# Optimization experiments

Hardware: AMD Instinct MI355X
Metric: run time of the kernel (lower is better)

Reference implementation:

```python
import jax, jax.numpy as jnp
import numpy as np

NUM_HEAD = 8

def conv1x1(x, W, b):
    # x: (n, c, h, w); W: (o, c); b: (o,)
    return jnp.einsum('nchw,oc->nohw', x, W) + b[None, :, None, None]

def setup_inputs() -> dict:
    key = jax.random.key(0)
    ks = jax.random.split(key, 9)
    n, C, H, Wd = 16, 512, 64, 64
    KC, VC = 256, 512
    s = lambda fan_in: 1.0 / np.sqrt(fan_in)
    return {
        'x':  jax.random.normal(ks[0], (n, C, H, Wd), dtype=jnp.float32),
        'Wk': jax.random.normal(ks[1], (KC, C), dtype=jnp.float32) * s(C),
        'bk': jnp.zeros((KC,), dtype=jnp.float32),
        'Wq': jax.random.normal(ks[2], (KC, C), dtype=jnp.float32) * s(C),
        'bq': jnp.zeros((KC,), dtype=jnp.float32),
        'Wv': jax.random.normal(ks[3], (VC, C), dtype=jnp.float32) * s(C),
        'bv': jnp.zeros((VC,), dtype=jnp.float32),
        'We': jax.random.normal(ks[4], (C, VC), dtype=jnp.float32) * s(VC),
        'be': jnp.zeros((C,), dtype=jnp.float32),
    }

def reference(x, Wk, bk, Wq, bq, Wv, bv, We, be):
    n, c, h, w = x.shape
    L = h * w
    Hn = NUM_HEAD
    key   = conv1x1(x, Wk, bk).reshape(n, Hn, -1, L)   # (n, H, hk, L)
    query = conv1x1(x, Wq, bq).reshape(n, Hn, -1, L)   # (n, H, hk, L)
    value = conv1x1(x, Wv, bv).reshape(n, Hn, -1, L)   # (n, H, hv, L)
    key_sm   = jax.nn.softmax(key, axis=3)              # softmax over spatial
    query_sm = jax.nn.softmax(query, axis=2)            # softmax over head channels
    # linear attention: (value @ key^T) @ query, no LxL matrix
    context = jnp.einsum('nhvl,nhkl->nhvk', value, key_sm)     # (n, H, hv, hk)
    att = jnp.einsum('nhvk,nhkl->nhvl', context, query_sm)     # (n, H, hv, L)
    att = att.reshape(n, -1, h, w)                              # (n, VC, h, w)
    return x + conv1x1(att, We, be)
```

## Files before the change

kernel.cpp:

```cpp
#include <hip/hip_runtime.h>
#include <cstddef>
#include <cstdint>

#define N_BATCH 16
#define C_IN    512
#define L       4096
#define KC      256
#define VC      512
#define NH      8
#define HK      32
#define HV      64

using f32x4 = __attribute__((ext_vector_type(4))) float;
using s16x8 = __attribute__((ext_vector_type(8))) short;

static __device__ inline ushort f2bf(float f) {
  uint32_t u = __float_as_uint(f);
  uint32_t r = (u + 0x7FFFu + ((u >> 16) & 1u)) >> 16;
  return (ushort)r;
}
static __device__ inline float bf2f(ushort u) {
  return __uint_as_float((uint32_t)u << 16);
}

__global__ __launch_bounds__(256) void k_prep_w(
    const float* __restrict__ Wk, const float* __restrict__ bk,
    const float* __restrict__ Wq, const float* __restrict__ bq,
    ushort* __restrict__ Wb, float* __restrict__ bb)
{
  const int o = blockIdx.x;
  const float* src; const float* bsrc; int oo;
  if (o < 256) { src = Wk + (size_t)o * C_IN;         bsrc = bk; oo = o; }
  else         { src = Wq + (size_t)(o - 256) * C_IN; bsrc = bq; oo = o - 256; }
  const int t = threadIdx.x;
  Wb[(size_t)o * C_IN + t * 2]     = f2bf(src[t * 2]);
  Wb[(size_t)o * C_IN + t * 2 + 1] = f2bf(src[t * 2 + 1]);
  if (t == 0) bb[o] = bsrc[oo];
}

__global__ __launch_bounds__(256) void k_prep_x(const float* __restrict__ x,
                                                ushort* __restrict__ xT)
{
  __shared__ float t[64][65];
  const int n = blockIdx.z, cy = blockIdx.y, lx = blockIdx.x;
  const float* xp = x + ((size_t)n * C_IN + cy * 64) * L + (size_t)lx * 64;
  const int l4 = (threadIdx.x & 15) * 4;
  const int c0 = threadIdx.x >> 4;
  #pragma unroll
  for (int i = 0; i < 4; ++i) {
    int cc = c0 + i * 16;
    f32x4 v = *(const f32x4*)&xp[(size_t)cc * L + l4];
    t[cc][l4]     = v[0];
    t[cc][l4 + 1] = v[1];
    t[cc][l4 + 2] = v[2];
    t[cc][l4 + 3] = v[3];
  }
  __syncthreads();
  ushort* op = xT + ((size_t)n * L + lx * 64) * C_IN + cy * 64;
  const int cp = (threadIdx.x & 15) * 4;
  const int l0 = threadIdx.x >> 4;
  #pragma unroll
  for (int i = 0; i < 4; ++i) {
    int lr = l0 + i * 16;
    uint2 pk;
    pk.x = (uint32_t)f2bf(t[cp][lr])     | ((uint32_t)f2bf(t[cp + 1][lr]) << 16);
    pk.y = (uint32_t)f2bf(t[cp + 2][lr]) | ((uint32_t)f2bf(t[cp + 3][lr]) << 16);
    *(uint2*)(op + (size_t)lr * C_IN + cp) = pk;
  }
}

#define QBM 256
#define QBN 256
#define QBK 64

__global__ __launch_bounds__(512) void k_kq_mfma(
    const ushort* __restrict__ Wb,
    const ushort* __restrict__ xT,
    const float* __restrict__ bb,
    ushort* __restrict__ Kbuf,
    ushort* __restrict__ qT)
{
  extern __shared__ __align__(16) char smem[];
  const int n  = blockIdx.z;
  const int oy = blockIdx.y;
  const int lx = blockIdx.x;
  const int tid  = threadIdx.x;
  const int wave = tid >> 6, lane = tid & 63;
  const int wr = wave >> 2, wc = wave & 3;

  f32x4 acc[8][4] = {};

  const ushort* gA = Wb + (size_t)(oy * QBM) * C_IN;
  const ushort* gB = xT + ((size_t)n * L + lx * QBN) * C_IN;

  const int srow = lane >> 3;
  const int sslotbase = lane & 7;

  #define QSTAGE(buf, k0)                                                        \
    {                                                                            \
      ushort* As_ = (ushort*)(smem + (buf) * 65536);                             \
      ushort* Bs_ = (ushort*)(smem + (buf) * 65536 + 32768);                     \
      _Pragma("unroll")                                                          \
      for (int i_ = 0; i_ < 4; ++i_) {                                           \
        int rbase_ = wave * 32 + i_ * 8;                                         \
        int row_ = rbase_ + srow;                                                \
        int ss_ = sslotbase ^ (row_ & 7);                                        \
        __builtin_amdgcn_global_load_lds(                                        \
            (const __attribute__((address_space(1))) uint32_t*)(gA + (size_t)row_ * C_IN + (k0) + ss_ * 8), \
            (__attribute__((address_space(3))) uint32_t*)(As_ + rbase_ * QBK),   \
            16, 0, 0);                                                           \
        __builtin_amdgcn_global_load_lds(                                        \
            (const __attribute__((address_space(1))) uint32_t*)(gB + (size_t)row_ * C_IN + (k0) + ss_ * 8), \
            (__attribute__((address_space(3))) uint32_t*)(Bs_ + rbase_ * QBK),   \
            16, 0, 0);                                                           \
      }                                                                          \
    }

  QSTAGE(0, 0)
  __syncthreads();

  const int nt = C_IN / QBK;
  for (int t = 0; t < nt; ++t) {
    if (t < nt - 1) QSTAGE((t + 1) & 1, (t + 1) * QBK)
    ushort* As = (ushort*)(smem + (t & 1) * 65536);
    ushort* Bs = (ushort*)(smem + (t & 1) * 65536 + 32768);
    __builtin_amdgcn_s_setprio(1);
    #pragma unroll
    for (int ks = 0; ks < 2; ++ks) {
      s16x8 af[8], bfr[4];
      #pragma unroll
      for (int m = 0; m < 8; ++m) {
        int row = wr * 128 + m * 16 + (lane & 15);
        int slot = (ks * 4 + (lane >> 4)) ^ (row & 7);
        af[m] = *(const s16x8*)&As[row * QBK + slot * 8];
      }
      #pragma unroll
      for (int nn = 0; nn < 4; ++nn) {
        int row = wc * 64 + nn * 16 + (lane & 15);
        int slot = (ks * 4 + (lane >> 4)) ^ (row & 7);
        bfr[nn] = *(const s16x8*)&Bs[row * QBK + slot * 8];
      }
      #pragma unroll
      for (int m = 0; m < 8; ++m)
        #pragma unroll
        for (int nn = 0; nn < 4; ++nn)
          acc[m][nn] = __builtin_amdgcn_mfma_f32_16x16x32_bf16(af[m], bfr[nn], acc[m][nn], 0, 0, 0);
    }
    __builtin_amdgcn_s_setprio(0);
    __syncthreads();
  }
  #undef QSTAGE

  if (oy == 0) {
    float* ep = (float*)smem + wave * (16 * 68);
    const int erow = lane >> 4;
    const int ecol = lane & 15;
    const float* bias = bb + wr * 128;
    ushort* outp = Kbuf + ((size_t)n * 256 + wr * 128) * L
                 + (size_t)lx * QBN + wc * 64;
    #pragma unroll
    for (int m = 0; m < 8; ++m) {
      #pragma unroll
      for (int nn = 0; nn < 4; ++nn)
        #pragma unroll
        for (int r = 0; r < 4; ++r)
          ep[(erow * 4 + r) * 68 + nn * 16 + ecol] = acc[m][nn][r];
      #pragma unroll
      for (int p = 0; p < 4; ++p) {
        int row = p * 4 + erow;
        f32x4 v = *(const f32x4*)&ep[row * 68 + ecol * 4];
        float bo = bias[m * 16 + row];
        uint2 pk;
        pk.x = (uint32_t)f2bf(v[0] + bo) | ((uint32_t)f2bf(v[1] + bo) << 16);
        pk.y = (uint32_t)f2bf(v[2] + bo) | ((uint32_t)f2bf(v[3] + bo) << 16);
        *(uint2*)&outp[(size_t)(m * 16 + row) * L + ecol * 4] = pk;
      }
    }
  } else {
    const float* bias = bb + 256 + wr * 128;
    ushort* qbase = qT + (size_t)n * L * KC;
    const int g4 = (lane >> 4) * 4;
    #pragma unroll
    for (int hp = 0; hp < 4; ++hp) {
      const int m0 = 2 * hp, m1 = 2 * hp + 1;
      const float b0_0 = bias[m0 * 16 + g4 + 0], b0_1 = bias[m0 * 16 + g4 + 1];
      const float b0_2 = bias[m0 * 16 + g4 + 2], b0_3 = bias[m0 * 16 + g4 + 3];
      const float b1_0 = bias[m1 * 16 + g4 + 0], b1_1 = bias[m1 * 16 + g4 + 1];
      const float b1_2 = bias[m1 * 16 + g4 + 2], b1_3 = bias[m1 * 16 + g4 + 3];
      #pragma unroll
      for (int nn = 0; nn < 4; ++nn) {
        float v0[4], v1[4];
        v0[0] = acc[m0][nn][0] + b0_0; v0[1] = acc[m0][nn][1] + b0_1;
        v0[2] = acc[m0][nn][2] + b0_2; v0[3] = acc[m0][nn][3] + b0_3;
        v1[0] = acc[m1][nn][0] + b1_0; v1[1] = acc[m1][nn][1] + b1_1;
        v1[2] = acc[m1][nn][2] + b1_2; v1[3] = acc[m1][nn][3] + b1_3;
        float mx = fmaxf(fmaxf(fmaxf(v0[0], v0[1]), fmaxf(v0[2], v0[3])),
                         fmaxf(fmaxf(v1[0], v1[1]), fmaxf(v1[2], v1[3])));
        mx = fmaxf(mx, __shfl_xor(mx, 16));
        mx = fmaxf(mx, __shfl_xor(mx, 32));
        float e0[4], e1[4];
        float s = 0.f;
        #pragma unroll
        for (int r = 0; r < 4; ++r) { e0[r] = __expf(v0[r] - mx); s += e0[r]; }
        #pragma unroll
        for (int r = 0; r < 4; ++r) { e1[r] = __expf(v1[r] - mx); s += e1[r]; }
        s += __shfl_xor(s, 16);
        s += __shfl_xor(s, 32);
        float inv = 1.0f / s;
        int l = lx * QBN + wc * 64 + nn * 16 + (lane & 15);
        ushort* dst = qbase + (size_t)l * KC + wr * 128;
        uint2 p0, p1;
        p0.x = (uint32_t)f2bf(e0[0] * inv) | ((uint32_t)f2bf(e0[1] * inv) << 16);
        p0.y = (uint32_t)f2bf(e0[2] * inv) | ((uint32_t)f2bf(e0[3] * inv) << 16);
        p1.x = (uint32_t)f2bf(e1[0] * inv) | ((uint32_t)f2bf(e1[1] * inv) << 16);
        p1.y = (uint32_t)f2bf(e1[2] * inv) | ((uint32_t)f2bf(e1[3] * inv) << 16);
        *(uint2*)&dst[m0 * 16 + g4] = p0;
        *(uint2*)&dst[m1 * 16 + g4] = p1;
      }
    }
  }
}

__device__ inline float blockReduceMax(float v, float* red) {
  #pragma unroll
  for (int off = 32; off > 0; off >>= 1)
    v = fmaxf(v, __shfl_down(v, off, 64));
  int tid = threadIdx.x;
  if ((tid & 63) == 0) red[tid >> 6] = v;
  __syncthreads();
  return fmaxf(fmaxf(red[0], red[1]), fmaxf(red[2], red[3]));
}
__device__ inline float blockReduceSum(float v, float* red) {
  #pragma unroll
  for (int off = 32; off > 0; off >>= 1)
    v += __shfl_down(v, off, 64);
  int tid = threadIdx.x;
  if ((tid & 63) == 0) red[tid >> 6] = v;
  __syncthreads();
  return red[0] + red[1] + red[2] + red[3];
}

__global__ __launch_bounds__(256) void k_kstats2(const ushort* __restrict__ Kbuf,
                                                 ushort* __restrict__ Ksm)
{
  const int r = blockIdx.x;
  const int n = blockIdx.y;
  const ushort* row = Kbuf + ((size_t)n * 256 + r) * L;
  ushort* orow = Ksm + ((size_t)n * 256 + r) * L;
  __shared__ float red1[4];
  __shared__ float red2[4];
  const int tid = threadIdx.x;
  s16x8 a = *(const s16x8*)(row + tid * 16);
  s16x8 b = *(const s16x8*)(row + tid * 16 + 8);
  float v[16];
  #pragma unroll
  for (int j = 0; j < 8; ++j) { v[j] = bf2f((ushort)a[j]); v[8 + j] = bf2f((ushort)b[j]); }
  float m = -3.0e38f;
  #pragma unroll
  for (int j = 0; j < 16; ++j) m = fmaxf(m, v[j]);
  m = blockReduceMax(m, red1);
  float s = 0.f;
  #pragma unroll
  for (int j = 0; j < 16; ++j) s += __expf(v[j] - m);
  s = blockReduceSum(s, red2);
  float inv = 1.0f / s;
  s16x8 w0, w1;
  #pragma unroll
  for (int j = 0; j < 8; ++j) {
    w0[j] = (short)f2bf(__expf(v[j] - m) * inv);
    w1[j] = (short)f2bf(__expf(v[8 + j] - m) * inv);
  }
  *(s16x8*)(orow + tid * 16)     = w0;
  *(s16x8*)(orow + tid * 16 + 8) = w1;
}

#define GBK 64

__global__ __launch_bounds__(512) void k_G(
    const float* __restrict__ x,
    const ushort* __restrict__ Ksm,
    float* __restrict__ Gp)
{
  extern __shared__ __align__(16) char smem[];
  const int cm = blockIdx.x;
  const int lc = blockIdx.y;
  const int n  = blockIdx.z;
  const int tid  = threadIdx.x;
  const int wave = tid >> 6, lane = tid & 63;
  const int wr = wave >> 2, wc = wave & 3;

  f32x4 acc[4][4] = {};

  const float*  gx = x   + ((size_t)n * C_IN + cm * 128) * L + lc * 1024;
  const ushort* gK = Ksm + (size_t)n * 256 * L + lc * 1024;

  const int arow = tid >> 2;
  const int aseg = (tid & 3) * 2;

  #define GSTAGEB(buf, k0)                                                       \
    {                                                                            \
      ushort* Bs_ = (ushort*)(smem + (buf) * 49152 + 16384);                     \
      _Pragma("unroll")                                                          \
      for (int i_ = 0; i_ < 4; ++i_) {                                           \
        int rbase_ = wave * 32 + i_ * 8;                                         \
        int row_ = rbase_ + (lane >> 3);                                         \
        int ss_ = (lane & 7) ^ (row_ & 7);                                       \
        __builtin_amdgcn_global_load_lds(                                        \
            (const __attribute__((address_space(1))) uint32_t*)(gK + (size_t)row_ * L + (k0) + ss_ * 8), \
            (__attribute__((address_space(3))) uint32_t*)(Bs_ + rbase_ * GBK),   \
            16, 0, 0);                                                           \
      }                                                                          \
    }

  #define GLOADA(k0)                                                             \
    a0 = *(const f32x4*)&gx[(size_t)arow * L + (k0) + aseg * 8];                 \
    a1 = *(const f32x4*)&gx[(size_t)arow * L + (k0) + aseg * 8 + 4];             \
    a2 = *(const f32x4*)&gx[(size_t)arow * L + (k0) + aseg * 8 + 8];             \
    a3 = *(const f32x4*)&gx[(size_t)arow * L + (k0) + aseg * 8 + 12];

  #define GWRITEA(buf)                                                           \
    {                                                                            \
      ushort* As_ = (ushort*)(smem + (buf) * 49152);                             \
      s16x8 w0_, w1_;                                                            \
      _Pragma("unroll")                                                          \
      for (int j_ = 0; j_ < 4; ++j_) {                                           \
        w0_[j_]     = (short)f2bf(a0[j_]);                                       \
        w0_[j_ + 4] = (short)f2bf(a1[j_]);                                       \
        w1_[j_]     = (short)f2bf(a2[j_]);                                       \
        w1_[j_ + 4] = (short)f2bf(a3[j_]);                                       \
      }                                                                          \
      *(s16x8*)&As_[arow * GBK + ((aseg)     ^ (arow & 7)) * 8] = w0_;           \
      *(s16x8*)&As_[arow * GBK + ((aseg + 1) ^ (arow & 7)) * 8] = w1_;           \
    }

  f32x4 a0, a1, a2, a3;

  GLOADA(0)
  GSTAGEB(0, 0)
  GWRITEA(0)
  __syncthreads();

  const int nt = 1024 / GBK;
  for (int t = 0; t < nt; ++t) {
    const int cb = t & 1, nb = cb ^ 1;
    if (t < nt - 1) {
      GLOADA((t + 1) * GBK)
      GSTAGEB(nb, (t + 1) * GBK)
    }
    ushort* As = (ushort*)(smem + cb * 49152);
    ushort* Bs = (ushort*)(smem + cb * 49152 + 16384);
    __builtin_amdgcn_s_setprio(1);
    #pragma unroll
    for (int ks = 0; ks < 2; ++ks) {
      s16x8 af[4], bfr[4];
      #pragma unroll
      for (int m = 0; m < 4; ++m) {
        int row = wr * 64 + m * 16 + (lane & 15);
        int slot = (ks * 4 + (lane >> 4)) ^ (row & 7);
        af[m] = *(const s16x8*)&As[row * GBK + slot * 8];
      }
      #pragma unroll
      for (int nn = 0; nn < 4; ++nn) {
        int row = wc * 64 + nn * 16 + (lane & 15);
        int slot = (ks * 4 + (lane >> 4)) ^ (row & 7);
        bfr[nn] = *(const s16x8*)&Bs[row * GBK + slot * 8];
      }
      #pragma unroll
      for (int m = 0; m < 4; ++m)
        #pragma unroll
        for (int nn = 0; nn < 4; ++nn)
          acc[m][nn] = __builtin_amdgcn_mfma_f32_16x16x32_bf16(af[m], bfr[nn], acc[m][nn], 0, 0, 0);
    }
    __builtin_amdgcn_s_setprio(0);
    if (t < nt - 1) GWRITEA(nb)
    __syncthreads();
  }
  #undef GSTAGEB
  #undef GLOADA
  #undef GWRITEA

  float* ep = (float*)smem + wave * (16 * 68);
  const int erow = lane >> 4;
  const int ecol = lane & 15;
  float* op = Gp + (((size_t)n * 4 + lc) * 512 + cm * 128 + wr * 64) * 256 + wc * 64;
  #pragma unroll
  for (int m = 0; m < 4; ++m) {
    #pragma unroll
    for (int nn = 0; nn < 4; ++nn)
      #pragma unroll
      for (int r = 0; r < 4; ++r)
        ep[(erow * 4 + r) * 68 + nn * 16 + ecol] = acc[m][nn][r];
    #pragma unroll
    for (int p = 0; p < 4; ++p) {
      int row16 = p * 4 + erow;
      f32x4 v = *(const f32x4*)&ep[row16 * 68 + ecol * 4];
      *(f32x4*)&op[(size_t)(m * 16 + row16) * 256 + ecol * 4] = v;
    }
  }
}

__global__ __launch_bounds__(256) void k_F(
    const float* __restrict__ Wv, const float* __restrict__ bv,
    const float* __restrict__ We,
    ushort* __restrict__ F, float* __restrict__ Fb)
{
  const int h  = blockIdx.x;
  const int og = blockIdx.y;
  const int tid = threadIdx.x;
  __shared__ float Ws[16][64];
  #pragma unroll
  for (int i = 0; i < 4; ++i) {
    int e = tid + i * 256;
    int o = e >> 6, v = e & 63;
    Ws[o][v] = We[(size_t)(og * 16 + o) * VC + h * 64 + v];
  }
  __syncthreads();
  const int c2 = tid * 2;
  float acc[16][2] = {};
  for (int v = 0; v < 64; ++v) {
    float2 w = *(const float2*)&Wv[(size_t)(h * 64 + v) * C_IN + c2];
    #pragma unroll
    for (int o = 0; o < 16; ++o) {
      acc[o][0] += Ws[o][v] * w.x;
      acc[o][1] += Ws[o][v] * w.y;
    }
  }
  ushort* Fh = F + ((size_t)h * 512 + og * 16) * C_IN;
  #pragma unroll
  for (int o = 0; o < 16; ++o) {
    uint32_t pk = (uint32_t)f2bf(acc[o][0]) | ((uint32_t)f2bf(acc[o][1]) << 16);
    *(uint32_t*)&Fh[(size_t)o * C_IN + c2] = pk;
  }
  if (tid < 16) {
    float s = 0.f;
    for (int v = 0; v < 64; ++v) s += Ws[tid][v] * bv[h * 64 + v];
    Fb[h * 512 + og * 16 + tid] = s;
  }
}

__global__ __launch_bounds__(256) void k_M(
    const float* __restrict__ Gp,
    const ushort* __restrict__ F,
    const float* __restrict__ Fb,
    ushort* __restrict__ Mbuf)
{
  const int oy = blockIdx.x;
  const int h  = blockIdx.y;
  const int n  = blockIdx.z;
  const int tid = threadIdx.x, wave = tid >> 6, lane = tid & 63;

  __shared__ __align__(16) char smem[32768 + 32768 + 9216];
  ushort* GTs = (ushort*)smem;

  #pragma unroll
  for (int i = 0; i < 16; ++i) {
    int e = tid + i * 256;
    int c = e >> 3, kq = e & 7;
    int k = kq * 4;
    const float* gp = Gp + ((size_t)n * 4 * 512 + c) * 256 + h * HK + k;
    f32x4 s = *(const f32x4*)gp;
    s += *(const f32x4*)(gp + (size_t)512 * 256);
    s += *(const f32x4*)(gp + (size_t)2 * 512 * 256);
    s += *(const f32x4*)(gp + (size_t)3 * 512 * 256);
    #pragma unroll
    for (int j = 0; j < 4; ++j) {
      int kk = k + j;
      GTs[kk * 512 + (((c >> 3) ^ (kk & 7)) * 8) + (c & 7)] = f2bf(s[j]);
    }
  }

  const ushort* gA = F + ((size_t)h * 512 + oy * 128) * C_IN;

  #define MSTAGE(buf, k0)                                                        \
    {                                                                            \
      ushort* As_ = (ushort*)(smem + 32768 + (buf) * 16384);                     \
      _Pragma("unroll")                                                          \
      for (int i_ = 0; i_ < 4; ++i_) {                                           \
        int rbase_ = wave * 32 + i_ * 8;                                         \
        int row_ = rbase_ + (lane >> 3);                                         \
        int ss_ = (lane & 7) ^ (row_ & 7);                                       \
        __builtin_amdgcn_global_load_lds(                                        \
            (const __attribute__((address_space(1))) uint32_t*)(gA + (size_t)row_ * C_IN + (k0) + ss_ * 8), \
            (__attribute__((address_space(3))) uint32_t*)(As_ + rbase_ * 64),    \
            16, 0, 0);                                                           \
      }                                                                          \
    }

  f32x4 acc[2][2] = {};

  MSTAGE(0, 0)
  __syncthreads();

  const int nt = C_IN / 64;
  for (int t = 0; t < nt; ++t) {
    if (t < nt - 1) MSTAGE((t + 1) & 1, (t + 1) * 64)
    ushort* As = (ushort*)(smem + 32768 + (t & 1) * 16384);
    __builtin_amdgcn_s_setprio(1);
    #pragma unroll
    for (int ks = 0; ks < 2; ++ks) {
      s16x8 af[2], bfr[2];
      #pragma unroll
      for (int m = 0; m < 2; ++m) {
        int row = wave * 32 + m * 16 + (lane & 15);
        int slot = (ks * 4 + (lane >> 4)) ^ (row & 7);
        af[m] = *(const s16x8*)&As[row * 64 + slot * 8];
      }
      #pragma unroll
      for (int nf = 0; nf < 2; ++nf) {
        int kr = nf * 16 + (lane & 15);
        int slot = (t * 8 + ks * 4 + (lane >> 4)) ^ (kr & 7);
        bfr[nf] = *(const s16x8*)&GTs[kr * 512 + slot * 8];
      }
      #pragma unroll
      for (int m = 0; m < 2; ++m)
        #pragma unroll
        for (int nf = 0; nf < 2; ++nf)
          acc[m][nf] = __builtin_amdgcn_mfma_f32_16x16x32_bf16(af[m], bfr[nf], acc[m][nf], 0, 0, 0);
    }
    __builtin_amdgcn_s_setprio(0);
    __syncthreads();
  }
  #undef MSTAGE

  float* ep = (float*)(smem + 65536) + wave * (16 * 36);
  const int erow = lane >> 4;
  const int ecol = lane & 15;
  #pragma unroll
  for (int m = 0; m < 2; ++m) {
    #pragma unroll
    for (int nf = 0; nf < 2; ++nf)
      #pragma unroll
      for (int r = 0; r < 4; ++r)
        ep[(erow * 4 + r) * 36 + nf * 16 + ecol] = acc[m][nf][r];
    #pragma unroll
    for (int p = 0; p < 2; ++p) {
      int row16 = p * 8 + (lane >> 3);
      int c4 = (lane & 7) * 4;
      f32x4 v = *(const f32x4*)&ep[row16 * 36 + c4];
      int o = oy * 128 + wave * 32 + m * 16 + row16;
      float fb = Fb[h * 512 + o];
      uint2 pk;
      pk.x = (uint32_t)f2bf(v[0] + fb) | ((uint32_t)f2bf(v[1] + fb) << 16);
      pk.y = (uint32_t)f2bf(v[2] + fb) | ((uint32_t)f2bf(v[3] + fb) << 16);
      *(uint2*)&Mbuf[((size_t)n * 512 + o) * KC + h * HK + c4] = pk;
    }
  }
}

#define BM 128
#define BN 128
#define BK 32

__global__ __launch_bounds__(256) void k_final_mfma(
    const ushort* __restrict__ Mb,
    const ushort* __restrict__ qT,
    const float* __restrict__ x,
    const float* __restrict__ be,
    float* __restrict__ out)
{
  const int n  = blockIdx.z;
  const int oy = blockIdx.y;
  const int lx = blockIdx.x;
  const int tid  = threadIdx.x;
  const int wave = tid >> 6, lane = tid & 63;
  const int wr = wave >> 1, wc = wave & 1;

  __shared__ __align__(16) char smem[32768 + 17408];

  f32x4 acc[4][4] = {};

  const ushort* gA = Mb + ((size_t)n * 512 + oy * BM) * KC;
  const ushort* gB = qT + ((size_t)n * L + lx * BN) * KC;

  const int r0 = wave * 32;
  const int lrow = lane >> 2;

  #define FSTAGE(buf, k0)                                                        \
    {                                                                            \
      ushort* As_ = (ushort*)(smem + (buf) * 16384);                             \
      ushort* Bs_ = (ushort*)(smem + (buf) * 16384 + 8192);                      \
      _Pragma("unroll")                                                          \
      for (int i_ = 0; i_ < 2; ++i_) {                                           \
        int row_ = r0 + i_ * 16 + lrow;                                          \
        int ss_ = (lane & 3) ^ ((row_ >> 1) & 3);                                \
        __builtin_amdgcn_global_load_lds(                                        \
            (const __attribute__((address_space(1))) uint32_t*)(gA + (size_t)row_ * KC + (k0) + ss_ * 8), \
            (__attribute__((address_space(3))) uint32_t*)(As_ + (r0 + i_ * 16) * BK), \
            16, 0, 0);                                                           \
        __builtin_amdgcn_global_load_lds(                                        \
            (const __attribute__((address_space(1))) uint32_t*)(gB + (size_t)row_ * KC + (k0) + ss_ * 8), \
            (__attribute__((address_space(3))) uint32_t*)(Bs_ + (r0 + i_ * 16) * BK), \
            16, 0, 0);                                                           \
      }                                                                          \
    }

  FSTAGE(0, 0)
  __syncthreads();

  const int nt = KC / BK;
  for (int t = 0; t < nt; ++t) {
    if (t < nt - 1) FSTAGE((t + 1) & 1, (t + 1) * BK)
    ushort* As = (ushort*)(smem + (t & 1) * 16384);
    ushort* Bs = (ushort*)(smem + (t & 1) * 16384 + 8192);
    s16x8 af[4], bfr[4];
    #pragma unroll
    for (int m = 0; m < 4; ++m) {
      int row = wr * 64 + m * 16 + (lane & 15);
      int slot = (lane >> 4) ^ ((row >> 1) & 3);
      af[m] = *(const s16x8*)&As[row * BK + slot * 8];
    }
    #pragma unroll
    for (int nn = 0; nn < 4; ++nn) {
      int row = wc * 64 + nn * 16 + (lane & 15);
      int slot = (lane >> 4) ^ ((row >> 1) & 3);
      bfr[nn] = *(const s16x8*)&Bs[row * BK + slot * 8];
    }
    __builtin_amdgcn_s_setprio(1);
    #pragma unroll
    for (int m = 0; m < 4; ++m)
      #pragma unroll
      for (int nn = 0; nn < 4; ++nn)
        acc[m][nn] = __builtin_amdgcn_mfma_f32_16x16x32_bf16(af[m], bfr[nn], acc[m][nn], 0, 0, 0);
    __builtin_amdgcn_s_setprio(0);
    __syncthreads();
  }
  #undef FSTAGE

  float* ep = (float*)(smem + 32768) + wave * (16 * 68);
  const int erow = lane >> 4;
  const int ecol = lane & 15;
  const float* bias = be + oy * BM + wr * 64;
  const float* xp = x + ((size_t)n * 512 + oy * BM + wr * 64) * L
                  + (size_t)lx * BN + wc * 64;
  float* op = out + ((size_t)n * 512 + oy * BM + wr * 64) * L
            + (size_t)lx * BN + wc * 64;
  #pragma unroll
  for (int m = 0; m < 4; ++m) {
    #pragma unroll
    for (int nn = 0; nn < 4; ++nn)
      #pragma unroll
      for (int r = 0; r < 4; ++r)
        ep[(erow * 4 + r) * 68 + nn * 16 + ecol] = acc[m][nn][r];
    #pragma unroll
    for (int p = 0; p < 4; ++p) {
      int row = p * 4 + erow;
      f32x4 v = *(const f32x4*)&ep[row * 68 + ecol * 4];
      float bo = bias[m * 16 + row];
      f32x4 xv = *(const f32x4*)&xp[(size_t)(m * 16 + row) * L + ecol * 4];
      v = v + xv + bo;
      *(f32x4*)&op[(size_t)(m * 16 + row) * L + ecol * 4] = v;
    }
  }
}

extern "C" void kernel_launch(void* const* d_in, const int* in_sizes, int n_in,
                              void* d_out, int out_size, void* d_ws, size_t ws_size,
                              hipStream_t stream)
{
  const float* x  = (const float*)d_in[0];
  const float* Wk = (const float*)d_in[1];
  const float* bk = (const float*)d_in[2];
  const float* Wq = (const float*)d_in[3];
  const float* bq = (const float*)d_in[4];
  const float* Wv = (const float*)d_in[5];
  const float* bv = (const float*)d_in[6];
  const float* We = (const float*)d_in[7];
  const float* be = (const float*)d_in[8];
  float* out = (float*)d_out;

  char* ws = (char*)d_ws;
  size_t off = 0;
  ushort* Kbuf = (ushort*)(ws + off); off += (size_t)N_BATCH * 256 * L * 2;
  ushort* Ksm  = (ushort*)(ws + off); off += (size_t)N_BATCH * 256 * L * 2;
  ushort* xT   = (ushort*)(ws + off); off += (size_t)N_BATCH * L * C_IN * 2;
  ushort* Wb   = (ushort*)(ws + off); off += (size_t)512 * C_IN * 2;
  float*  bb   = (float*)(ws + off);  off += (size_t)512 * 4;
  ushort* qT   = (ushort*)(ws + off); off += (size_t)N_BATCH * L * KC * 2;
  float*  Gp   = (float*)(ws + off);  off += (size_t)N_BATCH * 4 * 512 * 256 * 4;
  ushort* Fbuf = (ushort*)(ws + off); off += (size_t)NH * 512 * C_IN * 2;
  float*  Fb   = (float*)(ws + off);  off += (size_t)NH * 512 * 4;
  ushort* Mbuf = (ushort*)(ws + off); off += (size_t)N_BATCH * 512 * KC * 2;

  (void)hipFuncSetAttribute((const void*)k_kq_mfma,
                            hipFuncAttributeMaxDynamicSharedMemorySize, 131072);
  (void)hipFuncSetAttribute((const void*)k_G,
                            hipFuncAttributeMaxDynamicSharedMemorySize, 98304);

  k_prep_w<<<dim3(512), 256, 0, stream>>>(Wk, bk, Wq, bq, Wb, bb);
  k_F<<<dim3(NH, 32), 256, 0, stream>>>(Wv, bv, We, Fbuf, Fb);
  k_prep_x<<<dim3(64, 8, N_BATCH), 256, 0, stream>>>(x, xT);
  k_kq_mfma<<<dim3(16, 2, N_BATCH), 512, 131072, stream>>>(Wb, xT, bb, Kbuf, qT);
  k_kstats2<<<dim3(KC, N_BATCH), 256, 0, stream>>>(Kbuf, Ksm);
  k_G<<<dim3(4, 4, N_BATCH), 512, 98304, stream>>>(x, Ksm, Gp);
  k_M<<<dim3(4, NH, N_BATCH), 256, 0, stream>>>(Gp, Fbuf, Fb, Mbuf);
  k_final_mfma<<<dim3(32, 4, N_BATCH), 256, 0, stream>>>(Mbuf, qT, x, be, out);
}
```

Before: 265.7 us.

## Fuse key softmax normalization into G GEMM loads and stage bf16 x

```diff
diff --git a/kernel.cpp b/kernel.cpp
--- a/kernel.cpp
+++ b/kernel.cpp
@@ -39,11 +39,13 @@
 }
 
 __global__ __launch_bounds__(256) void k_prep_x(const float* __restrict__ x,
-                                                ushort* __restrict__ xT)
+                                                ushort* __restrict__ xT,
+                                                ushort* __restrict__ xb)
 {
   __shared__ float t[64][65];
   const int n = blockIdx.z, cy = blockIdx.y, lx = blockIdx.x;
   const float* xp = x + ((size_t)n * C_IN + cy * 64) * L + (size_t)lx * 64;
+  ushort* xbp = xb + ((size_t)n * C_IN + cy * 64) * L + (size_t)lx * 64;
   const int l4 = (threadIdx.x & 15) * 4;
   const int c0 = threadIdx.x >> 4;
   #pragma unroll
@@ -54,6 +56,10 @@
     t[cc][l4 + 1] = v[1];
     t[cc][l4 + 2] = v[2];
     t[cc][l4 + 3] = v[3];
+    uint2 pk;
+    pk.x = (uint32_t)f2bf(v[0]) | ((uint32_t)f2bf(v[1]) << 16);
+    pk.y = (uint32_t)f2bf(v[2]) | ((uint32_t)f2bf(v[3]) << 16);
+    *(uint2*)(xbp + (size_t)cc * L + l4) = pk;
   }
   __syncthreads();
   ushort* op = xT + ((size_t)n * L + lx * 64) * C_IN + cy * 64;
@@ -240,13 +246,13 @@
   return red[0] + red[1] + red[2] + red[3];
 }
 
-__global__ __launch_bounds__(256) void k_kstats2(const ushort* __restrict__ Kbuf,
-                                                 ushort* __restrict__ Ksm)
+__global__ __launch_bounds__(256) void k_kstats3(const ushort* __restrict__ Kbuf,
+                                                 float* __restrict__ kmax,
+                                                 float* __restrict__ kinv)
 {
   const int r = blockIdx.x;
   const int n = blockIdx.y;
   const ushort* row = Kbuf + ((size_t)n * 256 + r) * L;
-  ushort* orow = Ksm + ((size_t)n * 256 + r) * L;
   __shared__ float red1[4];
   __shared__ float red2[4];
   const int tid = threadIdx.x;
@@ -263,22 +269,16 @@
   #pragma unroll
   for (int j = 0; j < 16; ++j) s += __expf(v[j] - m);
   s = blockReduceSum(s, red2);
-  float inv = 1.0f / s;
-  s16x8 w0, w1;
-  #pragma unroll
-  for (int j = 0; j < 8; ++j) {
-    w0[j] = (short)f2bf(__expf(v[j] - m) * inv);
-    w1[j] = (short)f2bf(__expf(v[8 + j] - m) * inv);
-  }
-  *(s16x8*)(orow + tid * 16)     = w0;
-  *(s16x8*)(orow + tid * 16 + 8) = w1;
+  if (tid == 0) { kmax[n * KC + r] = m; kinv[n * KC + r] = 1.0f / s; }
 }
 
 #define GBK 64
 
 __global__ __launch_bounds__(512) void k_G(
-    const float* __restrict__ x,
-    const ushort* __restrict__ Ksm,
+    const ushort* __restrict__ xb,
+    const ushort* __restrict__ Kbuf,
+    const float* __restrict__ kmax,
+    const float* __restrict__ kinv,
     float* __restrict__ Gp)
 {
   extern __shared__ __align__(16) char smem[];
@@ -291,61 +291,60 @@
 
   f32x4 acc[4][4] = {};
 
-  const float*  gx = x   + ((size_t)n * C_IN + cm * 128) * L + lc * 1024;
-  const ushort* gK = Ksm + (size_t)n * 256 * L + lc * 1024;
-
-  const int arow = tid >> 2;
-  const int aseg = (tid & 3) * 2;
-
-  #define GSTAGEB(buf, k0)                                                       \
+  const ushort* gxb = xb   + ((size_t)n * C_IN + cm * 128) * L + lc * 1024;
+  const ushort* gK  = Kbuf + (size_t)n * 256 * L + lc * 1024;
+
+  const int brow = tid >> 1;
+  const int bseg0 = (tid & 1) * 4;
+  const float mk = kmax[n * KC + brow];
+  const float ik = kinv[n * KC + brow];
+
+  #define ASTAGE(buf, k0)                                                        \
+    {                                                                            \
+      ushort* As_ = (ushort*)(smem + (buf) * 49152);                             \
+      _Pragma("unroll")                                                          \
+      for (int i_ = 0; i_ < 2; ++i_) {                                           \
+        int rbase_ = wave * 16 + i_ * 8;                                         \
+        int row_ = rbase_ + (lane >> 3);                                         \
+        int ss_ = (lane & 7) ^ (row_ & 7);                                       \
+        __builtin_amdgcn_global_load_lds(                                        \
+            (const __attribute__((address_space(1))) uint32_t*)(gxb + (size_t)row_ * L + (k0) + ss_ * 8), \
+            (__attribute__((address_space(3))) uint32_t*)(As_ + rbase_ * GBK),   \
+            16, 0, 0);                                                           \
+      }                                                                          \
+    }
+
+  #define BLOAD(k0)                                                              \
+    _Pragma("unroll")                                                            \
+    for (int i_ = 0; i_ < 4; ++i_)                                               \
+      bk[i_] = *(const s16x8*)(gK + (size_t)brow * L + (k0) + (bseg0 + i_) * 8);
+
+  #define BWRITE(buf)                                                            \
     {                                                                            \
       ushort* Bs_ = (ushort*)(smem + (buf) * 49152 + 16384);                     \
       _Pragma("unroll")                                                          \
       for (int i_ = 0; i_ < 4; ++i_) {                                           \
-        int rbase_ = wave * 32 + i_ * 8;                                         \
-        int row_ = rbase_ + (lane >> 3);                                         \
-        int ss_ = (lane & 7) ^ (row_ & 7);                                       \
-        __builtin_amdgcn_global_load_lds(                                        \
-            (const __attribute__((address_space(1))) uint32_t*)(gK + (size_t)row_ * L + (k0) + ss_ * 8), \
-            (__attribute__((address_space(3))) uint32_t*)(Bs_ + rbase_ * GBK),   \
-            16, 0, 0);                                                           \
+        s16x8 w_;                                                                \
+        _Pragma("unroll")                                                        \
+        for (int j_ = 0; j_ < 8; ++j_)                                           \
+          w_[j_] = (short)f2bf(__expf(bf2f((ushort)bk[i_][j_]) - mk) * ik);      \
+        *(s16x8*)&Bs_[brow * GBK + ((bseg0 + i_) ^ (brow & 7)) * 8] = w_;        \
       }                                                                          \
     }
 
-  #define GLOADA(k0)                                                             \
-    a0 = *(const f32x4*)&gx[(size_t)arow * L + (k0) + aseg * 8];                 \
-    a1 = *(const f32x4*)&gx[(size_t)arow * L + (k0) + aseg * 8 + 4];             \
-    a2 = *(const f32x4*)&gx[(size_t)arow * L + (k0) + aseg * 8 + 8];             \
-    a3 = *(const f32x4*)&gx[(size_t)arow * L + (k0) + aseg * 8 + 12];
-
-  #define GWRITEA(buf)                                                           \
-    {                                                                            \
-      ushort* As_ = (ushort*)(smem + (buf) * 49152);                             \
-      s16x8 w0_, w1_;                                                            \
-      _Pragma("unroll")                                                          \
-      for (int j_ = 0; j_ < 4; ++j_) {                                           \
-        w0_[j_]     = (short)f2bf(a0[j_]);                                       \
-        w0_[j_ + 4] = (short)f2bf(a1[j_]);                                       \
-        w1_[j_]     = (short)f2bf(a2[j_]);                                       \
-        w1_[j_ + 4] = (short)f2bf(a3[j_]);                                       \
-      }                                                                          \
-      *(s16x8*)&As_[arow * GBK + ((aseg)     ^ (arow & 7)) * 8] = w0_;           \
-      *(s16x8*)&As_[arow * GBK + ((aseg + 1) ^ (arow & 7)) * 8] = w1_;           \
-    }
-
-  f32x4 a0, a1, a2, a3;
-
-  GLOADA(0)
-  GSTAGEB(0, 0)
-  GWRITEA(0)
+  s16x8 bk[4];
+
+  BLOAD(0)
+  ASTAGE(0, 0)
+  BWRITE(0)
   __syncthreads();
 
   const int nt = 1024 / GBK;
   for (int t = 0; t < nt; ++t) {
     const int cb = t & 1, nb = cb ^ 1;
     if (t < nt - 1) {
-      GLOADA((t + 1) * GBK)
-      GSTAGEB(nb, (t + 1) * GBK)
+      BLOAD((t + 1) * GBK)
+      ASTAGE(nb, (t + 1) * GBK)
     }
     ushort* As = (ushort*)(smem + cb * 49152);
     ushort* Bs = (ushort*)(smem + cb * 49152 + 16384);
@@ -372,12 +371,12 @@
           acc[m][nn] = __builtin_amdgcn_mfma_f32_16x16x32_bf16(af[m], bfr[nn], acc[m][nn], 0, 0, 0);
     }
     __builtin_amdgcn_s_setprio(0);
-    if (t < nt - 1) GWRITEA(nb)
+    if (t < nt - 1) BWRITE(nb)
     __syncthreads();
   }
-  #undef GSTAGEB
-  #undef GLOADA
-  #undef GWRITEA
+  #undef ASTAGE
+  #undef BLOAD
+  #undef BWRITE
 
   float* ep = (float*)smem + wave * (16 * 68);
   const int erow = lane >> 4;
@@ -671,10 +670,12 @@
   char* ws = (char*)d_ws;
   size_t off = 0;
   ushort* Kbuf = (ushort*)(ws + off); off += (size_t)N_BATCH * 256 * L * 2;
-  ushort* Ksm  = (ushort*)(ws + off); off += (size_t)N_BATCH * 256 * L * 2;
   ushort* xT   = (ushort*)(ws + off); off += (size_t)N_BATCH * L * C_IN * 2;
+  ushort* xb   = (ushort*)(ws + off); off += (size_t)N_BATCH * C_IN * L * 2;
   ushort* Wb   = (ushort*)(ws + off); off += (size_t)512 * C_IN * 2;
   float*  bb   = (float*)(ws + off);  off += (size_t)512 * 4;
+  float*  kmax = (float*)(ws + off);  off += (size_t)N_BATCH * KC * 4;
+  float*  kinv = (float*)(ws + off);  off += (size_t)N_BATCH * KC * 4;
   ushort* qT   = (ushort*)(ws + off); off += (size_t)N_BATCH * L * KC * 2;
   float*  Gp   = (float*)(ws + off);  off += (size_t)N_BATCH * 4 * 512 * 256 * 4;
   ushort* Fbuf = (ushort*)(ws + off); off += (size_t)NH * 512 * C_IN * 2;
@@ -688,10 +689,10 @@
 
   k_prep_w<<<dim3(512), 256, 0, stream>>>(Wk, bk, Wq, bq, Wb, bb);
   k_F<<<dim3(NH, 32), 256, 0, stream>>>(Wv, bv, We, Fbuf, Fb);
-  k_prep_x<<<dim3(64, 8, N_BATCH), 256, 0, stream>>>(x, xT);
+  k_prep_x<<<dim3(64, 8, N_BATCH), 256, 0, stream>>>(x, xT, xb);
   k_kq_mfma<<<dim3(16, 2, N_BATCH), 512, 131072, stream>>>(Wb, xT, bb, Kbuf, qT);
-  k_kstats2<<<dim3(KC, N_BATCH), 256, 0, stream>>>(Kbuf, Ksm);
-  k_G<<<dim3(4, 4, N_BATCH), 512, 98304, stream>>>(x, Ksm, Gp);
+  k_kstats3<<<dim3(KC, N_BATCH), 256, 0, stream>>>(Kbuf, kmax, kinv);
+  k_G<<<dim3(4, 4, N_BATCH), 512, 98304, stream>>>(xb, Kbuf, kmax, kinv, Gp);
   k_M<<<dim3(4, NH, N_BATCH), 256, 0, stream>>>(Gp, Fbuf, Fb, Mbuf);
   k_final_mfma<<<dim3(32, 4, N_BATCH), 256, 0, stream>>>(Mbuf, qT, x, be, out);
 }
```

New measurement: 268.0 us. About the same (+0.9%).
